# Kernel optimization log

Measured on AMD Instinct MI355X. Metric: run time of the kernel, lower is better.

## Reference

```python
import jax, jax.numpy as jnp
import numpy as np

N = 100000   # nodes
E = 1600000  # edges (avg degree 16)
F = 64       # conv_out_dim (= in_channels here)
EDGE_DIM = 16
B = 64       # graphs in batch
DEG = np.array([0, 1000, 2000, 4000, 8000, 16000, 24000, 20000, 12000, 6000, 3000, 2000, 1000, 500, 300, 200, 100], dtype=np.float64)
AVG_LOG = float((np.log(np.arange(len(DEG)) + 1.0) * DEG).sum() / DEG.sum())  # avg_deg['log']

def setup_inputs() -> dict:
    key = jax.random.key(0)
    ks = jax.random.split(key, 16)
    def w(k, shape, fan_in):
        return (jax.random.normal(k, shape, jnp.float32) / np.sqrt(fan_in)).astype(jnp.float32)
    return {
        "x": jax.random.normal(ks[0], (N, F), jnp.float32),
        "edge_attr": jax.random.normal(ks[1], (E, EDGE_DIM), jnp.float32),
        "edge_index": jax.random.randint(ks[2], (2, E), 0, N, jnp.int32),
        "batch": jnp.sort(jax.random.randint(ks[3], (N,), 0, B, jnp.int32)),
        # pre_mlp: Linear(F, F//2) -> ReLU -> Linear(F//2, F)
        "W1": w(ks[4], (F, F // 2), F), "b1": jnp.zeros((F // 2,), jnp.float32),
        "W2": w(ks[5], (F // 2, F), F // 2), "b2": jnp.zeros((F,), jnp.float32),
        # CEALConv (PNA-style) params
        "We": w(ks[6], (EDGE_DIM, F), EDGE_DIM), "be": jnp.zeros((F,), jnp.float32),   # edge encoder
        "Wp": w(ks[7], (3 * F, F), 3 * F), "bp": jnp.zeros((F,), jnp.float32),          # pre_nn
        "Wo": w(ks[8], (13 * F, F), 13 * F), "bo": jnp.zeros((F,), jnp.float32),        # post_nn ((4 agg * 3 scalers + 1) * F)
        "Wl": w(ks[9], (F, F), F), "bl": jnp.zeros((F,), jnp.float32),                  # final lin
        # BatchNorm affine
        "gamma": jnp.ones((F,), jnp.float32), "beta": jnp.zeros((F,), jnp.float32),
        # post_mlp: Linear(F, 100) -> ReLU -> Linear(100, 1)
        "Wm1": w(ks[10], (F, 100), F), "bm1": jnp.zeros((100,), jnp.float32),
        "Wm2": w(ks[11], (100, 1), 100), "bm2": jnp.zeros((1,), jnp.float32),
    }

def reference(x, edge_attr, edge_index, batch, W1, b1, W2, b2, We, be, Wp, bp, Wo, bo, Wl, bl, gamma, beta, Wm1, bm1, Wm2, bm2):
    src, dst = edge_index[0], edge_index[1]
    # pre-MLP on node features
    x = jax.nn.relu(x @ W1 + b1) @ W2 + b2                                  # [N, F]
    # message: pre_nn(cat[x_i, x_j, edge_encoder(edge_attr)]) -- split Wp to avoid concat
    e = edge_attr @ We + be                                                 # [E, F]
    h = x[dst] @ Wp[:F] + x[src] @ Wp[F:2 * F] + e @ Wp[2 * F:] + bp        # [E, F]
    # multi-aggregator scatter (mean, min, max, std) at destination nodes
    cnt = jax.ops.segment_sum(jnp.ones((E,), h.dtype), dst, N)              # in-degree [N]
    d = jnp.maximum(cnt, 1.0)[:, None]
    mean = jax.ops.segment_sum(h, dst, N) / d
    mean2 = jax.ops.segment_sum(h * h, dst, N) / d
    std = jnp.sqrt(jax.nn.relu(mean2 - mean * mean) + 1e-5)
    has = (cnt > 0)[:, None]
    mn = jnp.where(has, jax.ops.segment_min(h, dst, N), 0.0)
    mx = jnp.where(has, jax.ops.segment_max(h, dst, N), 0.0)
    agg = jnp.concatenate([mean, mn, mx, std], axis=-1)                     # [N, 4F]
    # degree scalers: identity, amplification, attenuation
    amp = jnp.log(d + 1.0) / AVG_LOG
    scaled = jnp.concatenate([agg, agg * amp, agg / amp], axis=-1)          # [N, 12F]
    # post_nn(cat[x, scaled]) then final linear
    out = jnp.concatenate([x, scaled], axis=-1) @ Wo + bo                   # [N, F]
    out = out @ Wl + bl
    # BatchNorm (batch statistics) + ReLU
    mu = out.mean(axis=0)
    var = out.var(axis=0)
    out = (out - mu) * jax.lax.rsqrt(var + 1e-5) * gamma + beta
    out = jax.nn.relu(out)
    # global_add_pool over graphs, then post-MLP head
    pooled = jax.ops.segment_sum(out, batch, B)                             # [B, F]
    return jax.nn.relu(pooled @ Wm1 + bm1) @ Wm2 + bm2                      # [B, 1]
```

## Files before the change

### kernel.cpp

```cpp
#include <hip/hip_runtime.h>
#include <hip/hip_bf16.h>
#include <math.h>

#define NN 100000
#define NE 1600000
#define FF 64
#define NB 64
#define NSCAN_BLOCKS 391

__device__ __constant__ float AVG_LOG_F = 1.9595436f;

typedef short short8 __attribute__((ext_vector_type(8)));
typedef float f32x4 __attribute__((ext_vector_type(4)));

__device__ __forceinline__ void atomAddF(float* p, float v) {
    __hip_atomic_fetch_add(p, v, __ATOMIC_RELAXED, __HIP_MEMORY_SCOPE_AGENT);
}
__device__ __forceinline__ float bf2f(short v) {
    return __uint_as_float(((unsigned)(unsigned short)v) << 16);
}
__device__ __forceinline__ unsigned packbf2(float a, float b) {
    unsigned ua = (unsigned)(unsigned short)__bfloat16_as_short(__float2bfloat16(a));
    unsigned ub = (unsigned)(unsigned short)__bfloat16_as_short(__float2bfloat16(b));
    return ua | (ub << 16);
}
__device__ __forceinline__ unsigned lds_pair(const unsigned short* p) {
    unsigned u;
    __builtin_memcpy(&u, p, 4);
    return u;
}
__device__ __forceinline__ float dot2bf(unsigned a, unsigned b, float c) {
    float d;
    asm("v_dot2_f32_bf16 %0, %1, %2, %3" : "=v"(d) : "v"(a), "v"(b), "v"(c));
    return d;
}

__global__ void fold_weights(const float* __restrict__ Wo, const float* __restrict__ Wl,
                             const float* __restrict__ bo, const float* __restrict__ bl,
                             const float* __restrict__ We, const float* __restrict__ Wp,
                             const float* __restrict__ bp, const float* __restrict__ be,
                             __hip_bfloat16* __restrict__ Wtb,
                             unsigned* __restrict__ Wepp,
                             float* __restrict__ bpF, float* __restrict__ boF) {
    int t = blockIdx.x * blockDim.x + threadIdx.x;
    if (t < 832 * 64) {
        int k = t >> 6, f = t & 63;
        float acc = 0.f;
        for (int j = 0; j < 64; j++) acc += Wo[k * 64 + j] * Wl[j * 64 + f];
        Wtb[f * 832 + k] = __float2bfloat16(acc);
    } else if (t < 832 * 64 + 512) {
        int u = t - 832 * 64; int k2 = u >> 6, f = u & 63;
        float a0 = 0.f, a1 = 0.f;
        for (int j = 0; j < 64; j++) {
            float wp = Wp[(128 + j) * 64 + f];
            a0 += We[(2 * k2) * 64 + j] * wp;
            a1 += We[(2 * k2 + 1) * 64 + j] * wp;
        }
        Wepp[k2 * 64 + f] = packbf2(a0, a1);
    } else if (t < 832 * 64 + 512 + 64) {
        int f = t - (832 * 64 + 512);
        float acc = bl[f];
        for (int j = 0; j < 64; j++) acc += bo[j] * Wl[j * 64 + f];
        boF[f] = acc;
    } else if (t < 832 * 64 + 512 + 128) {
        int f = t - (832 * 64 + 512 + 64);
        float acc = bp[f];
        for (int j = 0; j < 64; j++) acc += be[j] * Wp[(128 + j) * 64 + f];
        bpF[f] = acc;
    }
}

__global__ __launch_bounds__(256) void node_pre(const float* __restrict__ x,
                                                const float* __restrict__ W1, const float* __restrict__ b1,
                                                const float* __restrict__ W2, const float* __restrict__ b2,
                                                const float* __restrict__ Wp,
                                                const int* __restrict__ ei, unsigned* __restrict__ cnt_i,
                                                float* __restrict__ x2, float* __restrict__ A,
                                                __hip_bfloat16* __restrict__ Bnb) {
    __shared__ unsigned short xs[4][64], ts[4][32], x2s[4][64];
    int tid = threadIdx.x;
    int w = tid >> 6, f = tid & 63;
    int fm = f & 31;

    int nthreads = gridDim.x * 256;
    for (int e = blockIdx.x * 256 + tid; e < NE; e += nthreads)
        atomicAdd(&cnt_i[ei[NE + e]], 1u);

    unsigned w1p[32], w2p[16], wp0p[32], wp1p[32];
    #pragma unroll
    for (int k2 = 0; k2 < 32; ++k2)
        w1p[k2] = packbf2(W1[(2 * k2) * 32 + fm], W1[(2 * k2 + 1) * 32 + fm]);
    #pragma unroll
    for (int k2 = 0; k2 < 16; ++k2)
        w2p[k2] = packbf2(W2[(2 * k2) * 64 + f], W2[(2 * k2 + 1) * 64 + f]);
    #pragma unroll
    for (int k2 = 0; k2 < 32; ++k2) {
        wp0p[k2] = packbf2(Wp[(2 * k2) * 64 + f], Wp[(2 * k2 + 1) * 64 + f]);
        wp1p[k2] = packbf2(Wp[4096 + (2 * k2) * 64 + f], Wp[4096 + (2 * k2 + 1) * 64 + f]);
    }
    float b1f = b1[fm], b2f = b2[f];

    int wid = blockIdx.x * 4 + w;
    int nw = gridDim.x * 4;
    for (int v = wid; v < NN; v += nw) {
        float xv = x[(size_t)v * 64 + f];
        xs[w][f] = (unsigned short)__bfloat16_as_short(__float2bfloat16(xv));
        float t = b1f;
        #pragma unroll
        for (int k2 = 0; k2 < 32; ++k2) t = dot2bf(lds_pair(&xs[w][2 * k2]), w1p[k2], t);
        t = fmaxf(t, 0.f);
        if (f < 32) ts[w][f] = (unsigned short)__bfloat16_as_short(__float2bfloat16(t));
        float acc2 = b2f;
        #pragma unroll
        for (int k2 = 0; k2 < 16; ++k2) acc2 = dot2bf(lds_pair(&ts[w][2 * k2]), w2p[k2], acc2);
        x2[(size_t)v * 64 + f] = acc2;
        x2s[w][f] = (unsigned short)__bfloat16_as_short(__float2bfloat16(acc2));
        float aa = 0.f, bb = 0.f;
        #pragma unroll
        for (int k2 = 0; k2 < 32; ++k2) {
            unsigned xq = lds_pair(&x2s[w][2 * k2]);
            aa = dot2bf(xq, wp0p[k2], aa);
            bb = dot2bf(xq, wp1p[k2], bb);
        }
        A[(size_t)v * 64 + f] = aa;
        Bnb[(size_t)v * 64 + f] = __float2bfloat16(bb);
    }
}

__global__ void scan_blocksum(const unsigned* __restrict__ cnt_i, unsigned* __restrict__ bsum) {
    __shared__ unsigned red[256];
    int t = blockIdx.x * 256 + threadIdx.x;
    unsigned c = (t < NN) ? cnt_i[t] : 0u;
    red[threadIdx.x] = c; __syncthreads();
    for (int s = 128; s > 0; s >>= 1) {
        if (threadIdx.x < s) red[threadIdx.x] += red[threadIdx.x + s];
        __syncthreads();
    }
    if (threadIdx.x == 0) bsum[blockIdx.x] = red[0];
}

__global__ void scan_top(const unsigned* __restrict__ bsum, unsigned* __restrict__ boff,
                         unsigned* __restrict__ start) {
    __shared__ unsigned sh[512];
    int t = threadIdx.x;
    unsigned v = (t < NSCAN_BLOCKS) ? bsum[t] : 0u;
    sh[t] = v; __syncthreads();
    for (int d = 1; d < 512; d <<= 1) {
        unsigned add = (t >= d) ? sh[t - d] : 0u;
        __syncthreads();
        sh[t] += add;
        __syncthreads();
    }
    if (t < NSCAN_BLOCKS) boff[t] = sh[t] - v;
    if (t == 0) start[NN] = NE;
}

__global__ __launch_bounds__(256) void scan_final_deg(const unsigned* __restrict__ cnt_i,
                                                      const unsigned* __restrict__ boff,
                                                      unsigned* __restrict__ start,
                                                      unsigned* __restrict__ bh,
                                                      unsigned* __restrict__ rank_g) {
    __shared__ unsigned sh[256];
    __shared__ unsigned short keys[256];
    int b = blockIdx.x, t = threadIdx.x;
    int v = b * 256 + t;
    unsigned c = (v < NN) ? cnt_i[v] : 0u;
    sh[t] = c;
    unsigned d = 0xFFFFu;
    if (v < NN) d = (c > 255u) ? 255u : c;
    keys[t] = (unsigned short)d;
    __syncthreads();
    for (int dd = 1; dd < 256; dd <<= 1) {
        unsigned add = (t >= dd) ? sh[t - dd] : 0u;
        __syncthreads();
        sh[t] += add;
        __syncthreads();
    }
    if (v < NN) start[v] = boff[b] + sh[t] - c;
    unsigned cnt = 0;
    #pragma unroll 8
    for (int i = 0; i < 256; ++i) cnt += (keys[i] == (unsigned short)t) ? 1u : 0u;
    bh[t * NSCAN_BLOCKS + b] = cnt;
    if (v < NN) {
        unsigned r = 0;
        for (int i = 0; i < t; ++i) r += (keys[i] == (unsigned short)d) ? 1u : 0u;
        rank_g[v] = r;
    }
}

__global__ __launch_bounds__(256) void deg_colscan(const unsigned* __restrict__ bh,
                                                   unsigned* __restrict__ bhoff) {
    __shared__ unsigned sh[256];
    int bin = threadIdx.x;
    unsigned s = 0;
    for (int b = 0; b < NSCAN_BLOCKS; ++b) s += bh[bin * NSCAN_BLOCKS + b];
    sh[bin] = s;
    __syncthreads();
    for (int d = 1; d < 256; d <<= 1) {
        unsigned add = (bin >= d) ? sh[bin - d] : 0u;
        __syncthreads();
        sh[bin] += add;
        __syncthreads();
    }
    unsigned run = sh[bin] - s;
    for (int b = 0; b < NSCAN_BLOCKS; ++b) {
        unsigned c = bh[bin * NSCAN_BLOCKS + b];
        bhoff[bin * NSCAN_BLOCKS + b] = run;
        run += c;
    }
}

__global__ __launch_bounds__(256) void deg_place(const unsigned* __restrict__ cnt_i,
                                                 const unsigned* __restrict__ bhoff,
                                                 const unsigned* __restrict__ rank_g,
                                                 int* __restrict__ perm) {
    int t0 = threadIdx.x, b = blockIdx.x;
    int t = b * 256 + t0;
    if (t < NN) {
        unsigned d = cnt_i[t];
        if (d > 255u) d = 255u;
        perm[bhoff[d * NSCAN_BLOCKS + b] + rank_g[t]] = t;
    }
}

__global__ void scatter_kernel(const int* __restrict__ ei, const float* __restrict__ ea,
                               const unsigned* __restrict__ start,
                               unsigned* __restrict__ cnt_i,
                               __hip_bfloat16* __restrict__ eab, int* __restrict__ src_s) {
    int t = blockIdx.x * blockDim.x + threadIdx.x;
    if (t == 0) {
        src_s[NE] = 0;
        short8 z = {0, 0, 0, 0, 0, 0, 0, 0};
        short8* p = (short8*)(eab + (size_t)NE * 16);
        p[0] = z; p[1] = z;
    }
    if (t < NE) {
        int d = ei[NE + t];
        unsigned old = atomicSub(&cnt_i[d], 1u);
        unsigned pos = start[d] + old - 1u;
        src_s[pos] = ei[t];
        const float4* s4 = (const float4*)(ea + (size_t)t * 16);
        float4 a = s4[0], b = s4[1], c = s4[2], e = s4[3];
        short8 o0, o1;
        o0[0] = (short)__bfloat16_as_short(__float2bfloat16(a.x));
        o0[1] = (short)__bfloat16_as_short(__float2bfloat16(a.y));
        o0[2] = (short)__bfloat16_as_short(__float2bfloat16(a.z));
        o0[3] = (short)__bfloat16_as_short(__float2bfloat16(a.w));
        o0[4] = (short)__bfloat16_as_short(__float2bfloat16(b.x));
        o0[5] = (short)__bfloat16_as_short(__float2bfloat16(b.y));
        o0[6] = (short)__bfloat16_as_short(__float2bfloat16(b.z));
        o0[7] = (short)__bfloat16_as_short(__float2bfloat16(b.w));
        o1[0] = (short)__bfloat16_as_short(__float2bfloat16(c.x));
        o1[1] = (short)__bfloat16_as_short(__float2bfloat16(c.y));
        o1[2] = (short)__bfloat16_as_short(__float2bfloat16(c.z));
        o1[3] = (short)__bfloat16_as_short(__float2bfloat16(c.w));
        o1[4] = (short)__bfloat16_as_short(__float2bfloat16(e.x));
        o1[5] = (short)__bfloat16_as_short(__float2bfloat16(e.y));
        o1[6] = (short)__bfloat16_as_short(__float2bfloat16(e.z));
        o1[7] = (short)__bfloat16_as_short(__float2bfloat16(e.w));
        short8* dst8 = (short8*)(eab + (size_t)pos * 16);
        dst8[0] = o0; dst8[1] = o1;
    }
}

__global__ __launch_bounds__(256) void agg_post_kernel(const __hip_bfloat16* __restrict__ eab,
                                                       const int* __restrict__ src_s,
                                                       const unsigned* __restrict__ start,
                                                       const int* __restrict__ perm,
                                                       const float* __restrict__ A,
                                                       const unsigned short* __restrict__ Bnb,
                                                       const float* __restrict__ x2,
                                                       const unsigned* __restrict__ Wepp, const float* __restrict__ bpF,
                                                       const __hip_bfloat16* __restrict__ Wtb,
                                                       const float* __restrict__ boF,
                                                       float* __restrict__ out_pre,
                                                       float* __restrict__ bnsum, float* __restrict__ bnsum2) {
    __shared__ __hip_bfloat16 As[16 * 840];
    __shared__ int pvs[16];
    int tid = threadIdx.x;
    int w = __builtin_amdgcn_readfirstlane(tid >> 6);
    int f = tid & 63;
    int base = blockIdx.x * 16;

    unsigned wcolp[8];
    #pragma unroll
    for (int k = 0; k < 8; k++) wcolp[k] = Wepp[k * 64 + f];
    float bpf = bpF[f];

    int vv[4]; unsigned s0[4]; int len[4], lim[4]; float av[4];
    float sA[4] = {0.f, 0.f, 0.f, 0.f}, s2A[4] = {0.f, 0.f, 0.f, 0.f};
    float mnA[4], mxA[4];
    int maxlen = 0;
    #pragma unroll
    for (int g = 0; g < 4; ++g) {
        int v = __builtin_amdgcn_readfirstlane(perm[base + g * 4 + w]);
        vv[g] = v;
        if (f == 0) pvs[g * 4 + w] = v;
        unsigned a = start[v], b = start[v + 1];
        s0[g] = a; len[g] = (int)(b - a);
        lim[g] = len[g] > 0 ? len[g] - 1 : 0;
        maxlen = max(maxlen, len[g]);
        av[g] = A[(size_t)v * 64 + f] + bpf;
        mnA[g] = INFINITY; mxA[g] = -INFINITY;
    }

    int sP0[4], sP1[4];
    float bnC0[4], bnC1[4];
    #pragma unroll
    for (int g = 0; g < 4; ++g) {
        int a0 = src_s[s0[g]];
        int a1 = src_s[s0[g] + (unsigned)min(1, lim[g])];
        bnC0[g] = bf2f((short)Bnb[((size_t)a0 << 6) + f]);
        bnC1[g] = bf2f((short)Bnb[((size_t)a1 << 6) + f]);
        sP0[g] = src_s[s0[g] + (unsigned)min(2, lim[g])];
        sP1[g] = src_s[s0[g] + (unsigned)min(3, lim[g])];
    }

    for (int j = 0; j < maxlen; j += 2) {
        int sN0[4], sN1[4];
        float bnN0[4], bnN1[4];
        unsigned e0[4][8], e1[4][8];
        #pragma unroll
        for (int g = 0; g < 4; ++g) {
            sN0[g] = src_s[s0[g] + (unsigned)min(j + 4, lim[g])];
            sN1[g] = src_s[s0[g] + (unsigned)min(j + 5, lim[g])];
            bnN0[g] = bf2f((short)Bnb[((size_t)sP0[g] << 6) + f]);
            bnN1[g] = bf2f((short)Bnb[((size_t)sP1[g] << 6) + f]);
            const unsigned* p0 = (const unsigned*)(eab + (size_t)(s0[g] + (unsigned)min(j, lim[g])) * 16);
            const unsigned* p1 = (const unsigned*)(eab + (size_t)(s0[g] + (unsigned)min(j + 1, lim[g])) * 16);
            #pragma unroll
            for (int k = 0; k < 8; ++k) { e0[g][k] = p0[k]; e1[g][k] = p1[k]; }
        }
        #pragma unroll
        for (int g = 0; g < 4; ++g) {
            float h = av[g] + bnC0[g];
            #pragma unroll
            for (int k = 0; k < 8; k++) h = dot2bf(e0[g][k], wcolp[k], h);
            bool valid = j < len[g];
            float hm = valid ? h : 0.f;
            sA[g] += hm; s2A[g] += hm * hm;
            mnA[g] = fminf(mnA[g], h);
            mxA[g] = fmaxf(mxA[g], h);
        }
        #pragma unroll
        for (int g = 0; g < 4; ++g) {
            float h = av[g] + bnC1[g];
            #pragma unroll
            for (int k = 0; k < 8; k++) h = dot2bf(e1[g][k], wcolp[k], h);
            bool valid = (j + 1) < len[g];
            float hm = valid ? h : 0.f;
            sA[g] += hm; s2A[g] += hm * hm;
            mnA[g] = fminf(mnA[g], h);
            mxA[g] = fmaxf(mxA[g], h);
        }
        #pragma unroll
        for (int g = 0; g < 4; ++g) {
            bnC0[g] = bnN0[g]; bnC1[g] = bnN1[g];
            sP0[g] = sN0[g];   sP1[g] = sN1[g];
        }
    }

    #pragma unroll
    for (int g = 0; g < 4; ++g) {
        int n = g * 4 + w;
        int v = vv[g];
        float c = (float)len[g];
        float d = fmaxf(c, 1.f);
        float inv = 1.f / d;
        float mean = sA[g] * inv, mean2 = s2A[g] * inv;
        float sd = sqrtf(fmaxf(mean2 - mean * mean, 0.f) + 1e-5f);
        bool has = len[g] > 0;
        float mn = has ? mnA[g] : 0.f;
        float mx = has ? mxA[g] : 0.f;
        float l = __logf(d + 1.f);
        float amp = l * (1.0f / 1.9595436f);
        float iamp = 1.9595436f / l;
        __hip_bfloat16* row = &As[n * 840];
        row[f]        = __float2bfloat16(x2[(size_t)v * 64 + f]);
        row[64 + f]   = __float2bfloat16(mean);
        row[128 + f]  = __float2bfloat16(mn);
        row[192 + f]  = __float2bfloat16(mx);
        row[256 + f]  = __float2bfloat16(sd);
        row[320 + f]  = __float2bfloat16(mean * amp);
        row[384 + f]  = __float2bfloat16(mn * amp);
        row[448 + f]  = __float2bfloat16(mx * amp);
        row[512 + f]  = __float2bfloat16(sd * amp);
        row[576 + f]  = __float2bfloat16(mean * iamp);
        row[640 + f]  = __float2bfloat16(mn * iamp);
        row[704 + f]  = __float2bfloat16(mx * iamp);
        row[768 + f]  = __float2bfloat16(sd * iamp);
    }
    __syncthreads();

    int m = f & 15, q = f >> 4;
    int fbase = w * 16;
    f32x4 acc = {0.f, 0.f, 0.f, 0.f};
    const __hip_bfloat16* arow = &As[m * 840 + q * 8];
    const __hip_bfloat16* brow = &Wtb[(size_t)(fbase + m) * 832 + q * 8];
    #pragma unroll
    for (int s = 0; s < 26; ++s) {
        short8 af = *(const short8*)(arow + s * 32);
        short8 bf = *(const short8*)(brow + s * 32);
        acc = __builtin_amdgcn_mfma_f32_16x16x32_bf16(af, bf, acc, 0, 0, 0);
    }

    float bof = boF[fbase + m];
    float p1 = 0.f, p2 = 0.f;
    #pragma unroll
    for (int r = 0; r < 4; ++r) {
        float vvv = acc[r] + bof;
        int vn = pvs[q * 4 + r];
        out_pre[(size_t)vn * 64 + fbase + m] = vvv;
        p1 += vvv; p2 += vvv * vvv;
    }
    p1 += __shfl_xor(p1, 16); p2 += __shfl_xor(p2, 16);
    p1 += __shfl_xor(p1, 32); p2 += __shfl_xor(p2, 32);
    if (f < 16) {
        atomAddF(&bnsum[fbase + f], p1);
        atomAddF(&bnsum2[fbase + f], p2);
    }
}

__global__ __launch_bounds__(256) void bn_pool(const float* __restrict__ out_pre, const int* __restrict__ batch,
                                               const float* __restrict__ bnsum, const float* __restrict__ bnsum2,
                                               const float* __restrict__ gamma, const float* __restrict__ beta,
                                               float* __restrict__ pooled) {
    __shared__ float red[256];
    int tid = threadIdx.x, f = tid & 63, q = tid >> 6;
    int base = blockIdx.x * 64;
    float mu = bnsum[f] * (1.0f / NN);
    float var = bnsum2[f] * (1.0f / NN) - mu * mu;
    float sc = gamma[f] * rsqrtf(var + 1e-5f);
    float sh = beta[f] - mu * sc;
    int b_first = batch[base < NN ? base : NN - 1];
    int last = base + 63; if (last >= NN) last = NN - 1;
    int b_last = batch[last];
    if (b_first == b_last) {
        float local = 0.f;
        for (int g = 0; g < 16; ++g) {
            int v = base + g * 4 + q;
            if (v < NN) local += fmaxf(out_pre[(size_t)v * 64 + f] * sc + sh, 0.f);
        }
        red[tid] = local;
        __syncthreads();
        if (tid < 64) atomAddF(&pooled[b_first * 64 + f], red[f] + red[f + 64] + red[f + 128] + red[f + 192]);
    } else {
        for (int g = 0; g < 16; ++g) {
            int v = base + g * 4 + q;
            if (v < NN) {
                float val = fmaxf(out_pre[(size_t)v * 64 + f] * sc + sh, 0.f);
                atomAddF(&pooled[batch[v] * 64 + f], val);
            }
        }
    }
}

__global__ void head_kernel(const float* __restrict__ pooled,
                            const float* __restrict__ Wm1, const float* __restrict__ bm1,
                            const float* __restrict__ Wm2, const float* __restrict__ bm2,
                            float* __restrict__ out) {
    __shared__ float ts[64][104];
    int tid = threadIdx.x;
    for (int t = tid; t < 64 * 100; t += 256) {
        int b = t / 100, j = t % 100;
        float acc = bm1[j];
        for (int k = 0; k < 64; k++) acc += pooled[b * 64 + k] * Wm1[k * 100 + j];
        ts[b][j] = fmaxf(acc, 0.f);
    }
    __syncthreads();
    if (tid < 64) {
        float acc = bm2[0];
        for (int j = 0; j < 100; j++) acc += ts[tid][j] * Wm2[j];
        out[tid] = acc;
    }
}

extern "C" void kernel_launch(void* const* d_in, const int* in_sizes, int n_in,
                              void* d_out, int out_size, void* d_ws, size_t ws_size,
                              hipStream_t stream) {
    const float* x    = (const float*)d_in[0];
    const float* ea   = (const float*)d_in[1];
    const int*   ei   = (const int*)d_in[2];
    const int*   batch= (const int*)d_in[3];
    const float* W1   = (const float*)d_in[4];
    const float* b1   = (const float*)d_in[5];
    const float* W2   = (const float*)d_in[6];
    const float* b2   = (const float*)d_in[7];
    const float* We   = (const float*)d_in[8];
    const float* be   = (const float*)d_in[9];
    const float* Wp   = (const float*)d_in[10];
    const float* bp   = (const float*)d_in[11];
    const float* Wo   = (const float*)d_in[12];
    const float* bo   = (const float*)d_in[13];
    const float* Wl   = (const float*)d_in[14];
    const float* bl   = (const float*)d_in[15];
    const float* gamma= (const float*)d_in[16];
    const float* beta = (const float*)d_in[17];
    const float* Wm1  = (const float*)d_in[18];
    const float* bm1  = (const float*)d_in[19];
    const float* Wm2  = (const float*)d_in[20];
    const float* bm2  = (const float*)d_in[21];

    float* ws = (float*)d_ws;
    constexpr size_t NF = (size_t)NN * 64;
    const size_t o_x2     = 0;
    const size_t o_B      = NF;
    const size_t o_A      = 2 * NF;
    const size_t o_outpre = 3 * NF;
    const size_t o_start  = 4 * NF;
    const size_t o_cnt_i  = o_start + 100016;
    const size_t o_bsum   = o_cnt_i + 100000;
    const size_t o_boff   = o_bsum + 512;
    const size_t o_perm   = o_boff + 512;
    const size_t o_eab    = o_perm + 100000;
    const size_t o_srcs   = o_eab + 12800016;
    const size_t o_Wtb    = o_srcs + 1600016;
    const size_t o_Wepp   = o_Wtb + 26624;
    const size_t o_bpF    = o_Wepp + 512;
    const size_t o_boF    = o_bpF + 64;
    const size_t o_pooled = o_boF + 64;
    const size_t o_bnsum  = o_pooled + 64 * 64;
    const size_t o_bnsum2 = o_bnsum + 64;

    unsigned* bhoff  = (unsigned*)(ws + o_outpre);
    unsigned* rank_g = (unsigned*)(ws + o_outpre + 100096);
    unsigned* bh     = (unsigned*)(ws + o_outpre + 200096);

    hipMemsetAsync(ws + o_cnt_i, 0, 100000 * sizeof(unsigned), stream);
    hipMemsetAsync(ws + o_pooled, 0, (64 * 64 + 128) * sizeof(float), stream);

    fold_weights<<<213, 256, 0, stream>>>(Wo, Wl, bo, bl, We, Wp, bp, be,
                                          (__hip_bfloat16*)(ws + o_Wtb), (unsigned*)(ws + o_Wepp),
                                          ws + o_bpF, ws + o_boF);
    node_pre<<<768, 256, 0, stream>>>(x, W1, b1, W2, b2, Wp,
                                      ei, (unsigned*)(ws + o_cnt_i),
                                      ws + o_x2, ws + o_A, (__hip_bfloat16*)(ws + o_B));
    scan_blocksum<<<NSCAN_BLOCKS, 256, 0, stream>>>((unsigned*)(ws + o_cnt_i), (unsigned*)(ws + o_bsum));
    scan_top<<<1, 512, 0, stream>>>((unsigned*)(ws + o_bsum), (unsigned*)(ws + o_boff),
                                    (unsigned*)(ws + o_start));
    scan_final_deg<<<NSCAN_BLOCKS, 256, 0, stream>>>((unsigned*)(ws + o_cnt_i), (unsigned*)(ws + o_boff),
                                                     (unsigned*)(ws + o_start), bh, rank_g);
    deg_colscan<<<1, 256, 0, stream>>>(bh, bhoff);
    deg_place<<<NSCAN_BLOCKS, 256, 0, stream>>>((const unsigned*)(ws + o_cnt_i), bhoff, rank_g,
                                                (int*)(ws + o_perm));
    scatter_kernel<<<6250, 256, 0, stream>>>(ei, ea, (const unsigned*)(ws + o_start),
                                             (unsigned*)(ws + o_cnt_i),
                                             (__hip_bfloat16*)(ws + o_eab), (int*)(ws + o_srcs));
    agg_post_kernel<<<6250, 256, 0, stream>>>((const __hip_bfloat16*)(ws + o_eab),
                                              (const int*)(ws + o_srcs),
                                              (const unsigned*)(ws + o_start),
                                              (const int*)(ws + o_perm),
                                              ws + o_A, (const unsigned short*)(ws + o_B), ws + o_x2,
                                              (const unsigned*)(ws + o_Wepp), ws + o_bpF,
                                              (const __hip_bfloat16*)(ws + o_Wtb), ws + o_boF,
                                              ws + o_outpre, ws + o_bnsum, ws + o_bnsum2);
    bn_pool<<<1563, 256, 0, stream>>>(ws + o_outpre, batch,
                                      ws + o_bnsum, ws + o_bnsum2, gamma, beta, ws + o_pooled);
    head_kernel<<<1, 256, 0, stream>>>(ws + o_pooled, Wm1, bm1, Wm2, bm2, (float*)d_out);
}
```

Measured before the change: 688.5 us.

## Fuse degree placement into scatter, transpose bin histogram, halve GEMM LDS tile

The degree-bucket histogram is stored block-major so the column-scan reads are coalesced. The separate deg_place kernel is folded into the scatter kernel, which computes degree from start offsets and writes perm in reversed order so high-degree nodes are scheduled first. The agg_post LDS A-tile is cut from 840 to 456 columns by building and consuming the 832-wide feature row in two halves with an extra barrier, which lowers LDS per block to allow higher occupancy. The cost is an additional sync and staging pass per block, and the scatter kernel now carries the placement work.

```diff
diff --git a/kernel.cpp b/kernel.cpp
--- a/kernel.cpp
+++ b/kernel.cpp
@@ -180,7 +180,7 @@
     unsigned cnt = 0;
     #pragma unroll 8
     for (int i = 0; i < 256; ++i) cnt += (keys[i] == (unsigned short)t) ? 1u : 0u;
-    bh[t * NSCAN_BLOCKS + b] = cnt;
+    bh[b * 256 + t] = cnt;
     if (v < NN) {
         unsigned r = 0;
         for (int i = 0; i < t; ++i) r += (keys[i] == (unsigned short)d) ? 1u : 0u;
@@ -193,7 +193,7 @@
     __shared__ unsigned sh[256];
     int bin = threadIdx.x;
     unsigned s = 0;
-    for (int b = 0; b < NSCAN_BLOCKS; ++b) s += bh[bin * NSCAN_BLOCKS + b];
+    for (int b = 0; b < NSCAN_BLOCKS; ++b) s += bh[b * 256 + bin];
     sh[bin] = s;
     __syncthreads();
     for (int d = 1; d < 256; d <<= 1) {
@@ -204,28 +204,18 @@
     }
     unsigned run = sh[bin] - s;
     for (int b = 0; b < NSCAN_BLOCKS; ++b) {
-        unsigned c = bh[bin * NSCAN_BLOCKS + b];
-        bhoff[bin * NSCAN_BLOCKS + b] = run;
+        unsigned c = bh[b * 256 + bin];
+        bhoff[b * 256 + bin] = run;
         run += c;
-    }
-}
-
-__global__ __launch_bounds__(256) void deg_place(const unsigned* __restrict__ cnt_i,
-                                                 const unsigned* __restrict__ bhoff,
-                                                 const unsigned* __restrict__ rank_g,
-                                                 int* __restrict__ perm) {
-    int t0 = threadIdx.x, b = blockIdx.x;
-    int t = b * 256 + t0;
-    if (t < NN) {
-        unsigned d = cnt_i[t];
-        if (d > 255u) d = 255u;
-        perm[bhoff[d * NSCAN_BLOCKS + b] + rank_g[t]] = t;
     }
 }
 
 __global__ void scatter_kernel(const int* __restrict__ ei, const float* __restrict__ ea,
                                const unsigned* __restrict__ start,
                                unsigned* __restrict__ cnt_i,
+                               const unsigned* __restrict__ bhoff,
+                               const unsigned* __restrict__ rank_g,
+                               int* __restrict__ perm,
                                __hip_bfloat16* __restrict__ eab, int* __restrict__ src_s) {
     int t = blockIdx.x * blockDim.x + threadIdx.x;
     if (t == 0) {
@@ -233,6 +223,12 @@
         short8 z = {0, 0, 0, 0, 0, 0, 0, 0};
         short8* p = (short8*)(eab + (size_t)NE * 16);
         p[0] = z; p[1] = z;
+    }
+    if (t < NN) {
+        unsigned d = start[t + 1] - start[t];
+        if (d > 255u) d = 255u;
+        unsigned pos = bhoff[(t >> 8) * 256 + d] + rank_g[t];
+        perm[NN - 1 - pos] = t;
     }
     if (t < NE) {
         int d = ei[NE + t];
@@ -275,7 +271,7 @@
                                                        const float* __restrict__ boF,
                                                        float* __restrict__ out_pre,
                                                        float* __restrict__ bnsum, float* __restrict__ bnsum2) {
-    __shared__ __hip_bfloat16 As[16 * 840];
+    __shared__ __hip_bfloat16 As[16 * 456];
     __shared__ int pvs[16];
     int tid = threadIdx.x;
     int w = __builtin_amdgcn_readfirstlane(tid >> 6);
@@ -360,47 +356,67 @@
         }
     }
 
+    float meanv[4], mnv[4], mxv[4], sdv[4], ampv[4], iampv[4];
     #pragma unroll
     for (int g = 0; g < 4; ++g) {
-        int n = g * 4 + w;
-        int v = vv[g];
         float c = (float)len[g];
         float d = fmaxf(c, 1.f);
         float inv = 1.f / d;
         float mean = sA[g] * inv, mean2 = s2A[g] * inv;
-        float sd = sqrtf(fmaxf(mean2 - mean * mean, 0.f) + 1e-5f);
+        sdv[g] = sqrtf(fmaxf(mean2 - mean * mean, 0.f) + 1e-5f);
         bool has = len[g] > 0;
-        float mn = has ? mnA[g] : 0.f;
-        float mx = has ? mxA[g] : 0.f;
+        meanv[g] = mean;
+        mnv[g] = has ? mnA[g] : 0.f;
+        mxv[g] = has ? mxA[g] : 0.f;
         float l = __logf(d + 1.f);
-        float amp = l * (1.0f / 1.9595436f);
-        float iamp = 1.9595436f / l;
-        __hip_bfloat16* row = &As[n * 840];
-        row[f]        = __float2bfloat16(x2[(size_t)v * 64 + f]);
-        row[64 + f]   = __float2bfloat16(mean);
-        row[128 + f]  = __float2bfloat16(mn);
-        row[192 + f]  = __float2bfloat16(mx);
-        row[256 + f]  = __float2bfloat16(sd);
-        row[320 + f]  = __float2bfloat16(mean * amp);
-        row[384 + f]  = __float2bfloat16(mn * amp);
-        row[448 + f]  = __float2bfloat16(mx * amp);
-        row[512 + f]  = __float2bfloat16(sd * amp);
-        row[576 + f]  = __float2bfloat16(mean * iamp);
-        row[640 + f]  = __float2bfloat16(mn * iamp);
-        row[704 + f]  = __float2bfloat16(mx * iamp);
-        row[768 + f]  = __float2bfloat16(sd * iamp);
+        ampv[g] = l * (1.0f / 1.9595436f);
+        iampv[g] = 1.9595436f / l;
+    }
+
+    #pragma unroll
+    for (int g = 0; g < 4; ++g) {
+        int n = g * 4 + w;
+        __hip_bfloat16* row = &As[n * 456];
+        row[f]        = __float2bfloat16(x2[(size_t)vv[g] * 64 + f]);
+        row[64 + f]   = __float2bfloat16(meanv[g]);
+        row[128 + f]  = __float2bfloat16(mnv[g]);
+        row[192 + f]  = __float2bfloat16(mxv[g]);
+        row[256 + f]  = __float2bfloat16(sdv[g]);
+        row[320 + f]  = __float2bfloat16(meanv[g] * ampv[g]);
+        row[384 + f]  = __float2bfloat16(mnv[g] * ampv[g]);
     }
     __syncthreads();
 
     int m = f & 15, q = f >> 4;
     int fbase = w * 16;
     f32x4 acc = {0.f, 0.f, 0.f, 0.f};
-    const __hip_bfloat16* arow = &As[m * 840 + q * 8];
+    const __hip_bfloat16* arow = &As[m * 456 + q * 8];
     const __hip_bfloat16* brow = &Wtb[(size_t)(fbase + m) * 832 + q * 8];
     #pragma unroll
-    for (int s = 0; s < 26; ++s) {
+    for (int s = 0; s < 14; ++s) {
         short8 af = *(const short8*)(arow + s * 32);
         short8 bf = *(const short8*)(brow + s * 32);
+        acc = __builtin_amdgcn_mfma_f32_16x16x32_bf16(af, bf, acc, 0, 0, 0);
+    }
+    __syncthreads();
+
+    #pragma unroll
+    for (int g = 0; g < 4; ++g) {
+        int n = g * 4 + w;
+        __hip_bfloat16* row = &As[n * 456];
+        row[f]        = __float2bfloat16(mxv[g] * ampv[g]);
+        row[64 + f]   = __float2bfloat16(sdv[g] * ampv[g]);
+        row[128 + f]  = __float2bfloat16(meanv[g] * iampv[g]);
+        row[192 + f]  = __float2bfloat16(mnv[g] * iampv[g]);
+        row[256 + f]  = __float2bfloat16(mxv[g] * iampv[g]);
+        row[320 + f]  = __float2bfloat16(sdv[g] * iampv[g]);
+    }
+    __syncthreads();
+
+    #pragma unroll
+    for (int s = 0; s < 12; ++s) {
+        short8 af = *(const short8*)(arow + s * 32);
+        short8 bf = *(const short8*)(brow + (14 + s) * 32);
         acc = __builtin_amdgcn_mfma_f32_16x16x32_bf16(af, bf, acc, 0, 0, 0);
     }
 
@@ -541,10 +557,9 @@
     scan_final_deg<<<NSCAN_BLOCKS, 256, 0, stream>>>((unsigned*)(ws + o_cnt_i), (unsigned*)(ws + o_boff),
                                                      (unsigned*)(ws + o_start), bh, rank_g);
     deg_colscan<<<1, 256, 0, stream>>>(bh, bhoff);
-    deg_place<<<NSCAN_BLOCKS, 256, 0, stream>>>((const unsigned*)(ws + o_cnt_i), bhoff, rank_g,
-                                                (int*)(ws + o_perm));
     scatter_kernel<<<6250, 256, 0, stream>>>(ei, ea, (const unsigned*)(ws + o_start),
                                              (unsigned*)(ws + o_cnt_i),
+                                             bhoff, rank_g, (int*)(ws + o_perm),
                                              (__hip_bfloat16*)(ws + o_eab), (int*)(ws + o_srcs));
     agg_post_kernel<<<6250, 256, 0, stream>>>((const __hip_bfloat16*)(ws + o_eab),
                                               (const int*)(ws + o_srcs),
```

After: 708.6 us. 1.03x slower.
